# Optimization experiments

Measured on AMD Instinct MI355X. Metric: run time of the kernel, lower is better.

## Reference

```python
import jax, jax.numpy as jnp
import numpy as np

EMB = 1024
HEADS = 16
DH = EMB // HEADS


def setup_inputs() -> dict:
    key = jax.random.key(0)
    ks = jax.random.split(key, 9)
    B, S = 4, 2048
    scale = 1.0 / np.sqrt(EMB)
    x = jax.random.normal(ks[0], (B, S, EMB), dtype=jnp.float32)
    Wq = jax.random.normal(ks[1], (EMB, EMB), dtype=jnp.float32) * scale
    Wk = jax.random.normal(ks[2], (EMB, EMB), dtype=jnp.float32) * scale
    Wv = jax.random.normal(ks[3], (EMB, EMB), dtype=jnp.float32) * scale
    Wo = jax.random.normal(ks[4], (EMB, EMB), dtype=jnp.float32) * scale
    bq = jnp.zeros((EMB,), jnp.float32)
    bk = jnp.zeros((EMB,), jnp.float32)
    bv = jnp.zeros((EMB,), jnp.float32)
    bo = jnp.zeros((EMB,), jnp.float32)
    return {"x": x, "Wq": Wq, "bq": bq, "Wk": Wk, "bk": bk,
            "Wv": Wv, "bv": bv, "Wo": Wo, "bo": bo}


def _split_heads(t):
    B, S, _ = t.shape
    return t.reshape(B, S, HEADS, DH).transpose(0, 2, 1, 3)  # [B,H,S,Dh]


def reference(x, Wq, bq, Wk, bk, Wv, bv, Wo, bo):
    q = _split_heads(x @ Wq + bq)
    k = _split_heads(x @ Wk + bk)
    v = _split_heads(x @ Wv + bv)
    # scaled dot-product attention, full [B,H,S,S] score matrix as in source
    logits = jnp.einsum("bhqd,bhkd->bhqk", q, k) / jnp.sqrt(jnp.float32(DH))
    attn = jax.nn.softmax(logits, axis=-1)
    ctx = jnp.einsum("bhqk,bhkd->bhqd", attn, v)
    B, _, S, _ = ctx.shape
    concat = ctx.transpose(0, 2, 1, 3).reshape(B, S, EMB)
    return concat @ Wo + bo
```

## Files before the change

### kernel.cpp

```cpp
#include <hip/hip_runtime.h>
#include <hip/hip_bf16.h>
#include <stdint.h>

typedef __bf16 bf16;
typedef __bf16 bf16x4 __attribute__((ext_vector_type(4)));
typedef __bf16 bf16x8 __attribute__((ext_vector_type(8)));
typedef float f32x4 __attribute__((ext_vector_type(4)));

__device__ __forceinline__ void async_ld16(const void* g, void* l) {
  __builtin_amdgcn_global_load_lds(
      (__attribute__((address_space(1))) void*)(void*)(g),
      (__attribute__((address_space(3))) void*)(l), 16, 0, 0);
}

__device__ __forceinline__ bf16 fast_bf16(float f) {
  uint32_t u = (__float_as_uint(f) + 0x8000u) >> 16;
  union { uint16_t s; bf16 b; } cv;
  cv.s = (uint16_t)u;
  return cv.b;
}

__device__ __forceinline__ uint32_t pack_bf16(float lo, float hi) {
  return __builtin_amdgcn_perm(__float_as_uint(hi) + 0x8000u,
                               __float_as_uint(lo) + 0x8000u, 0x07060302u);
}

__global__ __launch_bounds__(256) void cast_f32_bf16(const float* __restrict__ in,
                                                     bf16* __restrict__ out, int n) {
  int i = (blockIdx.x * 256 + threadIdx.x) * 4;
  if (i < n) {
    float4 f = *(const float4*)(in + i);
    uint2 o;
    o.x = pack_bf16(f.x, f.y);
    o.y = pack_bf16(f.z, f.w);
    *(uint2*)(out + i) = o;
  }
}

__global__ __launch_bounds__(256) void transpose_weights(const float* __restrict__ Wq,
                                                         const float* __restrict__ Wk,
                                                         const float* __restrict__ Wv,
                                                         const float* __restrict__ Wo,
                                                         bf16* __restrict__ Wt,
                                                         bf16* __restrict__ Wot) {
  __shared__ bf16 tile[64][66];
  int z = blockIdx.z;
  const float* src = z == 0 ? Wq : (z == 1 ? Wk : (z == 2 ? Wv : Wo));
  bf16* dst = z == 0 ? Wt : (z == 1 ? Wt + 1048576 : (z == 2 ? Wt + 2097152 : Wot));
  int r0 = blockIdx.x * 64, c0 = blockIdx.y * 64;
  int t = threadIdx.x;
#pragma unroll
  for (int i = 0; i < 16; ++i) {
    int idx = t + i * 256;
    int r = idx >> 6, c = idx & 63;
    tile[r][c] = fast_bf16(src[(size_t)(r0 + r) * 1024 + (c0 + c)]);
  }
  __syncthreads();
#pragma unroll
  for (int i = 0; i < 16; ++i) {
    int idx = t + i * 256;
    int c = idx >> 6, r = idx & 63;
    dst[(size_t)(c0 + c) * 1024 + (r0 + r)] = tile[r][c];
  }
}

__device__ __forceinline__ void gemm128_mainloop(const bf16* __restrict__ A,
                                                 const bf16* __restrict__ Bt, int K,
                                                 int rowBase, int colBase,
                                                 bf16* As, bf16* Bs,
                                                 f32x4 (&acc)[4][4]) {
  int t = threadIdx.x, lane = t & 63, w = t >> 6;
  int wM = w >> 1, wN = w & 1, quad = lane >> 4, l15 = lane & 15;
  int r_off = lane >> 3;
  int c_sw = (((lane & 7) ^ r_off) << 3);
  int sw = l15 & 7;
  for (int k0 = 0; k0 < K; k0 += 64) {
    __syncthreads();
#pragma unroll
    for (int i = 0; i < 4; ++i) {
      int e = i * 2048 + w * 512;
      int row = (e >> 6) + r_off;
      async_ld16(A + (size_t)(rowBase + row) * K + (k0 + c_sw), As + e);
      async_ld16(Bt + (size_t)(colBase + row) * K + (k0 + c_sw), Bs + e);
    }
    __syncthreads();
#pragma unroll
    for (int ks = 0; ks < 2; ++ks) {
      int co = (((ks * 4 + quad) ^ sw) << 3);
      bf16x8 af[4], bfr[4];
#pragma unroll
      for (int mi = 0; mi < 4; ++mi)
        af[mi] = *(const bf16x8*)(As + (wM * 64 + mi * 16 + l15) * 64 + co);
#pragma unroll
      for (int ni = 0; ni < 4; ++ni)
        bfr[ni] = *(const bf16x8*)(Bs + (wN * 64 + ni * 16 + l15) * 64 + co);
#pragma unroll
      for (int mi = 0; mi < 4; ++mi)
#pragma unroll
        for (int ni = 0; ni < 4; ++ni)
          acc[mi][ni] = __builtin_amdgcn_mfma_f32_16x16x32_bf16(af[mi], bfr[ni], acc[mi][ni], 0, 0, 0);
    }
  }
}

__global__ __launch_bounds__(256) void gemm_qkv(const bf16* __restrict__ X,
                                                const bf16* __restrict__ Wt,
                                                const float* __restrict__ bq,
                                                const float* __restrict__ bk,
                                                const float* __restrict__ bv,
                                                bf16* __restrict__ Qo,
                                                bf16* __restrict__ Ko,
                                                bf16* __restrict__ Vto) {
  __shared__ alignas(16) bf16 smem[2 * 128 * 64];
  bf16* As = smem;
  bf16* Bs = smem + 128 * 64;
  f32x4 acc[4][4];
  f32x4 z = {0.f, 0.f, 0.f, 0.f};
#pragma unroll
  for (int mi = 0; mi < 4; ++mi)
#pragma unroll
    for (int ni = 0; ni < 4; ++ni) acc[mi][ni] = z;
  int rowBase = blockIdx.x * 128, colBase = blockIdx.y * 128;
  gemm128_mainloop(X, Wt, 1024, rowBase, colBase, As, Bs, acc);

  int t = threadIdx.x, lane = t & 63, w = t >> 6;
  int wM = w >> 1, wN = w & 1, quad = lane >> 4, l15 = lane & 15;
  int which = colBase >> 10;

  if (which == 2) {
    int baseh = (colBase & 1023) >> 6;
    int b = rowBase >> 11, s0 = rowBase & 2047;
#pragma unroll
    for (int hp = 0; hp < 2; ++hp) {
      __syncthreads();
      if (wN == hp) {
#pragma unroll
        for (int mi = 0; mi < 4; ++mi)
#pragma unroll
          for (int ni = 0; ni < 4; ++ni) {
            int d = ni * 16 + l15;
            float bb = bv[(colBase & 1023) + hp * 64 + d];
            int sl = wM * 64 + mi * 16 + quad * 4;
            uint2 pv;
            pv.x = pack_bf16(acc[mi][ni][0] + bb, acc[mi][ni][1] + bb);
            pv.y = pack_bf16(acc[mi][ni][2] + bb, acc[mi][ni][3] + bb);
            *(uint2*)(smem + d * 136 + sl) = pv;
          }
      }
      __syncthreads();
      int hg = baseh + hp;
#pragma unroll
      for (int it = 0; it < 4; ++it) {
        int idx = t + it * 256;
        int d = idx >> 4, c = idx & 15;
        bf16x8 vv = *(const bf16x8*)(smem + d * 136 + c * 8);
        *(bf16x8*)(Vto + (((size_t)((b << 4) + hg) << 6) + d) * 2048 + s0 + c * 8) = vv;
      }
    }
  } else {
    const float* bias = which == 0 ? bq : bk;
    bf16* dst = which == 0 ? Qo : Ko;
    float scale = which == 0 ? 0.125f * 1.44269504f : 1.0f;
#pragma unroll
    for (int mi = 0; mi < 4; ++mi)
#pragma unroll
      for (int ni = 0; ni < 4; ++ni) {
        int n = colBase + wN * 64 + ni * 16 + l15;
        int e = n & 1023;
        int h = e >> 6, d = e & 63;
        float bb = bias[e];
#pragma unroll
        for (int r = 0; r < 4; ++r) {
          int m = rowBase + wM * 64 + mi * 16 + quad * 4 + r;
          int b = m >> 11, s = m & 2047;
          dst[(((size_t)((b << 4) + h) * 2048 + s) << 6) + d] =
              fast_bf16((acc[mi][ni][r] + bb) * scale);
        }
      }
  }
}

__global__ __launch_bounds__(256) void gemm_out(const bf16* __restrict__ Cb,
                                                const bf16* __restrict__ Wot,
                                                const float* __restrict__ bo,
                                                float* __restrict__ out) {
  __shared__ alignas(16) bf16 As[128 * 64];
  __shared__ alignas(16) bf16 Bs[128 * 64];
  f32x4 acc[4][4];
  f32x4 z = {0.f, 0.f, 0.f, 0.f};
#pragma unroll
  for (int mi = 0; mi < 4; ++mi)
#pragma unroll
    for (int ni = 0; ni < 4; ++ni) acc[mi][ni] = z;
  int rowBase = blockIdx.x * 128, colBase = blockIdx.y * 128;
  gemm128_mainloop(Cb, Wot, 1024, rowBase, colBase, As, Bs, acc);

  int t = threadIdx.x, lane = t & 63, w = t >> 6;
  int wM = w >> 1, wN = w & 1, quad = lane >> 4, l15 = lane & 15;
#pragma unroll
  for (int mi = 0; mi < 4; ++mi)
#pragma unroll
    for (int ni = 0; ni < 4; ++ni) {
      int n = colBase + wN * 64 + ni * 16 + l15;
      float bb = bo[n];
#pragma unroll
      for (int r = 0; r < 4; ++r) {
        int m = rowBase + wM * 64 + mi * 16 + quad * 4 + r;
        out[(size_t)m * 1024 + n] = acc[mi][ni][r] + bb;
      }
    }
}

__global__ __launch_bounds__(256, 2) void attn(const bf16* __restrict__ Q,
                                               const bf16* __restrict__ Kg,
                                               const bf16* __restrict__ Vt,
                                               bf16* __restrict__ ctx) {
  __shared__ alignas(16) bf16 KVs[4][4096];
  __shared__ alignas(16) bf16 Ps[4][2048];

  int t = threadIdx.x, lane = t & 63, w = t >> 6;
  int quad = lane >> 4, l15 = lane & 15;
  int r_off = lane >> 3;
  int c_sw = (((lane & 7) ^ r_off) << 3);
  int sw = l15 & 7;
  int bh = blockIdx.y;
  int q0 = blockIdx.x * 256;
  const bf16* Qp = Q + ((size_t)bh * 2048 + q0) * 64;
  const bf16* Kp = Kg + (size_t)bh * 2048 * 64;
  const bf16* Vp = Vt + (size_t)bh * 64 * 2048;

#pragma unroll
  for (int i = 0; i < 8; ++i) {
    int e = i * 512;
    int row = i * 8 + r_off;
    async_ld16(Qp + (size_t)(w * 64 + row) * 64 + c_sw, KVs[w] + e);
  }
  __syncthreads();

  bf16x8 qf[2][4];
#pragma unroll
  for (int ks = 0; ks < 2; ++ks)
#pragma unroll
    for (int qi = 0; qi < 4; ++qi)
      qf[ks][qi] = *(const bf16x8*)(KVs[w] + (qi * 16 + l15) * 64 + (((ks * 4 + quad) ^ sw) << 3));
  __syncthreads();

#pragma unroll
  for (int i = 0; i < 2; ++i) {
    int e = w * 1024 + i * 512;
    int row = (e >> 6) + r_off;
    async_ld16(Kp + (size_t)row * 64 + c_sw, KVs[0] + e);
    async_ld16(Vp + (size_t)row * 2048 + c_sw, KVs[2] + e);
  }

  bf16 one1 = (bf16)1.0f;
  bf16x8 ones = {one1, one1, one1, one1, one1, one1, one1, one1};
  bf16* Pw = Ps[w];

  f32x4 o[4][4];
  f32x4 ol[4];
  f32x4 z = {0.f, 0.f, 0.f, 0.f};
#pragma unroll
  for (int mi = 0; mi < 4; ++mi) {
    ol[mi] = z;
#pragma unroll
    for (int ni = 0; ni < 4; ++ni) o[mi][ni] = z;
  }

  for (int kt = 0; kt < 32; ++kt) {
    int cur = kt & 1;
    __syncthreads();
    if (kt < 31) {
      int kn = (kt + 1) * 64;
#pragma unroll
      for (int i = 0; i < 2; ++i) {
        int e = w * 1024 + i * 512;
        int row = (e >> 6) + r_off;
        async_ld16(Kp + (size_t)(kn + row) * 64 + c_sw, KVs[cur ^ 1] + e);
        async_ld16(Vp + (size_t)row * 2048 + kn + c_sw, KVs[2 + (cur ^ 1)] + e);
      }
    }
    const bf16* Kc = KVs[cur];
    const bf16* Vc = KVs[2 + cur];

    f32x4 sA[2][4];
#pragma unroll
    for (int ki = 0; ki < 2; ++ki)
#pragma unroll
      for (int qi = 0; qi < 4; ++qi) sA[ki][qi] = z;
#pragma unroll
    for (int ks = 0; ks < 2; ++ks) {
      int co = (((ks * 4 + quad) ^ sw) << 3);
      bf16x8 kf0 = *(const bf16x8*)(Kc + (l15)*64 + co);
      bf16x8 kf1 = *(const bf16x8*)(Kc + (16 + l15) * 64 + co);
#pragma unroll
      for (int qi = 0; qi < 4; ++qi) {
        sA[0][qi] = __builtin_amdgcn_mfma_f32_16x16x32_bf16(kf0, qf[ks][qi], sA[0][qi], 0, 0, 0);
        sA[1][qi] = __builtin_amdgcn_mfma_f32_16x16x32_bf16(kf1, qf[ks][qi], sA[1][qi], 0, 0, 0);
      }
    }
#pragma unroll
    for (int qi = 0; qi < 4; ++qi)
#pragma unroll
      for (int ki = 0; ki < 2; ++ki) {
        float p0 = __builtin_amdgcn_exp2f(sA[ki][qi][0]);
        float p1 = __builtin_amdgcn_exp2f(sA[ki][qi][1]);
        float p2 = __builtin_amdgcn_exp2f(sA[ki][qi][2]);
        float p3 = __builtin_amdgcn_exp2f(sA[ki][qi][3]);
        uint2 pb;
        pb.x = pack_bf16(p0, p1);
        pb.y = pack_bf16(p2, p3);
        *(uint2*)(Pw + (qi * 16 + l15) * 32 + ki * 16 + quad * 4) = pb;
      }

    f32x4 sB[2][4];
#pragma unroll
    for (int ki = 0; ki < 2; ++ki)
#pragma unroll
      for (int qi = 0; qi < 4; ++qi) sB[ki][qi] = z;
#pragma unroll
    for (int ks = 0; ks < 2; ++ks) {
      int co = (((ks * 4 + quad) ^ sw) << 3);
      bf16x8 kf2 = *(const bf16x8*)(Kc + (32 + l15) * 64 + co);
      bf16x8 kf3 = *(const bf16x8*)(Kc + (48 + l15) * 64 + co);
#pragma unroll
      for (int qi = 0; qi < 4; ++qi) {
        sB[0][qi] = __builtin_amdgcn_mfma_f32_16x16x32_bf16(kf2, qf[ks][qi], sB[0][qi], 0, 0, 0);
        sB[1][qi] = __builtin_amdgcn_mfma_f32_16x16x32_bf16(kf3, qf[ks][qi], sB[1][qi], 0, 0, 0);
      }
    }

    asm volatile("s_waitcnt lgkmcnt(0)" ::: "memory");

    {
      int co = ((quad ^ sw) << 3);
      bf16x8 pf[4], vf[4];
#pragma unroll
      for (int mi = 0; mi < 4; ++mi)
        pf[mi] = *(const bf16x8*)(Pw + (mi * 16 + l15) * 32 + quad * 8);
#pragma unroll
      for (int ni = 0; ni < 4; ++ni)
        vf[ni] = *(const bf16x8*)(Vc + (ni * 16 + l15) * 64 + co);
#pragma unroll
      for (int mi = 0; mi < 4; ++mi) {
#pragma unroll
        for (int ni = 0; ni < 4; ++ni)
          o[mi][ni] = __builtin_amdgcn_mfma_f32_16x16x32_bf16(pf[mi], vf[ni], o[mi][ni], 0, 0, 0);
        ol[mi] = __builtin_amdgcn_mfma_f32_16x16x32_bf16(pf[mi], ones, ol[mi], 0, 0, 0);
      }
    }

#pragma unroll
    for (int qi = 0; qi < 4; ++qi)
#pragma unroll
      for (int ki = 0; ki < 2; ++ki) {
        float p0 = __builtin_amdgcn_exp2f(sB[ki][qi][0]);
        float p1 = __builtin_amdgcn_exp2f(sB[ki][qi][1]);
        float p2 = __builtin_amdgcn_exp2f(sB[ki][qi][2]);
        float p3 = __builtin_amdgcn_exp2f(sB[ki][qi][3]);
        uint2 pb;
        pb.x = pack_bf16(p0, p1);
        pb.y = pack_bf16(p2, p3);
        *(uint2*)(Pw + (qi * 16 + l15) * 32 + ki * 16 + quad * 4) = pb;
      }

    asm volatile("s_waitcnt lgkmcnt(0)" ::: "memory");

    {
      int co = (((4 + quad) ^ sw) << 3);
      bf16x8 pf[4], vf[4];
#pragma unroll
      for (int mi = 0; mi < 4; ++mi)
        pf[mi] = *(const bf16x8*)(Pw + (mi * 16 + l15) * 32 + quad * 8);
#pragma unroll
      for (int ni = 0; ni < 4; ++ni)
        vf[ni] = *(const bf16x8*)(Vc + (ni * 16 + l15) * 64 + co);
#pragma unroll
      for (int mi = 0; mi < 4; ++mi) {
#pragma unroll
        for (int ni = 0; ni < 4; ++ni)
          o[mi][ni] = __builtin_amdgcn_mfma_f32_16x16x32_bf16(pf[mi], vf[ni], o[mi][ni], 0, 0, 0);
        ol[mi] = __builtin_amdgcn_mfma_f32_16x16x32_bf16(pf[mi], ones, ol[mi], 0, 0, 0);
      }
    }
  }

  int b = bh >> 4, h = bh & 15;
#pragma unroll
  for (int mi = 0; mi < 4; ++mi) {
    float rl[4];
#pragma unroll
    for (int r = 0; r < 4; ++r) rl[r] = 1.0f / ol[mi][r];
#pragma unroll
    for (int ni = 0; ni < 4; ++ni) {
      int col = h * 64 + ni * 16 + l15;
#pragma unroll
      for (int r = 0; r < 4; ++r) {
        int q = q0 + w * 64 + mi * 16 + quad * 4 + r;
        ctx[(size_t)(b * 2048 + q) * 1024 + col] = fast_bf16(o[mi][ni][r] * rl[r]);
      }
    }
  }
}

extern "C" void kernel_launch(void* const* d_in, const int* in_sizes, int n_in,
                              void* d_out, int out_size, void* d_ws, size_t ws_size,
                              hipStream_t stream) {
  const float* x  = (const float*)d_in[0];
  const float* Wq = (const float*)d_in[1];
  const float* bq = (const float*)d_in[2];
  const float* Wk = (const float*)d_in[3];
  const float* bk = (const float*)d_in[4];
  const float* Wv = (const float*)d_in[5];
  const float* bv = (const float*)d_in[6];
  const float* Wo = (const float*)d_in[7];
  const float* bo = (const float*)d_in[8];
  float* out = (float*)d_out;

  char* ws = (char*)d_ws;
  const size_t MB = 1048576;
  bf16* xb  = (bf16*)(ws);
  bf16* Wt  = (bf16*)(ws + 16 * MB);
  bf16* Wot = (bf16*)(ws + 22 * MB);
  bf16* Qb  = (bf16*)(ws + 24 * MB);
  bf16* Kb  = (bf16*)(ws + 40 * MB);
  bf16* Vtb = (bf16*)(ws + 56 * MB);
  bf16* Cx  = (bf16*)(ws + 72 * MB);

  cast_f32_bf16<<<8192, 256, 0, stream>>>(x, xb, 8388608);
  transpose_weights<<<dim3(16, 16, 4), 256, 0, stream>>>(Wq, Wk, Wv, Wo, Wt, Wot);
  gemm_qkv<<<dim3(64, 24, 1), 256, 0, stream>>>(xb, Wt, bq, bk, bv, Qb, Kb, Vtb);
  attn<<<dim3(8, 64, 1), 256, 0, stream>>>(Qb, Kb, Vtb, Cx);
  gemm_out<<<dim3(64, 8, 1), 256, 0, stream>>>(Cx, Wot, bo, out);
}
```

Baseline: 310.7 us.

## Stage Q/K epilogue through LDS, swap grid order, restructure attention LDS

The Q/K GEMM epilogue now stages each head tile in shared memory and writes 16-byte vectorized rows, replacing scattered 2-byte stores. All three kernels swap grid axes so consecutive blocks share the same row or head tile, which should improve L2 reuse. The attention kernel reuses the Q staging buffer for P with an XOR swizzle, loads the first K/V tile together with Q, and moves the per-iteration barrier to the end of the loop. LDS per block grows slightly, and occupancy may change.

```diff
diff --git a/kernel.cpp b/kernel.cpp
--- a/kernel.cpp
+++ b/kernel.cpp
@@ -120,16 +120,16 @@
   for (int mi = 0; mi < 4; ++mi)
 #pragma unroll
     for (int ni = 0; ni < 4; ++ni) acc[mi][ni] = z;
-  int rowBase = blockIdx.x * 128, colBase = blockIdx.y * 128;
+  int rowBase = blockIdx.y * 128, colBase = blockIdx.x * 128;
   gemm128_mainloop(X, Wt, 1024, rowBase, colBase, As, Bs, acc);
 
   int t = threadIdx.x, lane = t & 63, w = t >> 6;
   int wM = w >> 1, wN = w & 1, quad = lane >> 4, l15 = lane & 15;
   int which = colBase >> 10;
+  int baseh = (colBase & 1023) >> 6;
+  int b = rowBase >> 11, s0 = rowBase & 2047;
 
   if (which == 2) {
-    int baseh = (colBase & 1023) >> 6;
-    int b = rowBase >> 11, s0 = rowBase & 2047;
 #pragma unroll
     for (int hp = 0; hp < 2; ++hp) {
       __syncthreads();
@@ -162,21 +162,32 @@
     bf16* dst = which == 0 ? Qo : Ko;
     float scale = which == 0 ? 0.125f * 1.44269504f : 1.0f;
 #pragma unroll
-    for (int mi = 0; mi < 4; ++mi)
-#pragma unroll
-      for (int ni = 0; ni < 4; ++ni) {
-        int n = colBase + wN * 64 + ni * 16 + l15;
-        int e = n & 1023;
-        int h = e >> 6, d = e & 63;
-        float bb = bias[e];
-#pragma unroll
-        for (int r = 0; r < 4; ++r) {
-          int m = rowBase + wM * 64 + mi * 16 + quad * 4 + r;
-          int b = m >> 11, s = m & 2047;
-          dst[(((size_t)((b << 4) + h) * 2048 + s) << 6) + d] =
-              fast_bf16((acc[mi][ni][r] + bb) * scale);
-        }
-      }
+    for (int hp = 0; hp < 2; ++hp) {
+      __syncthreads();
+      if (wN == hp) {
+#pragma unroll
+        for (int mi = 0; mi < 4; ++mi)
+#pragma unroll
+          for (int ni = 0; ni < 4; ++ni) {
+            int d = ni * 16 + l15;
+            float bb = bias[(colBase & 1023) + hp * 64 + d];
+            int m = wM * 64 + mi * 16 + quad * 4;
+#pragma unroll
+            for (int r = 0; r < 4; ++r)
+              smem[(m + r) * 72 + d] = fast_bf16((acc[mi][ni][r] + bb) * scale);
+          }
+      }
+      __syncthreads();
+      int hg = baseh + hp;
+      bf16* gbase = dst + ((((size_t)((b << 4) + hg)) * 2048 + s0) << 6);
+#pragma unroll
+      for (int it = 0; it < 4; ++it) {
+        int idx = t + it * 256;
+        int m = idx >> 3, c = idx & 7;
+        bf16x8 vv = *(const bf16x8*)(smem + m * 72 + c * 8);
+        *(bf16x8*)(gbase + m * 64 + c * 8) = vv;
+      }
+    }
   }
 }
 
@@ -192,7 +203,7 @@
   for (int mi = 0; mi < 4; ++mi)
 #pragma unroll
     for (int ni = 0; ni < 4; ++ni) acc[mi][ni] = z;
-  int rowBase = blockIdx.x * 128, colBase = blockIdx.y * 128;
+  int rowBase = blockIdx.y * 128, colBase = blockIdx.x * 128;
   gemm128_mainloop(Cb, Wot, 1024, rowBase, colBase, As, Bs, acc);
 
   int t = threadIdx.x, lane = t & 63, w = t >> 6;
@@ -215,47 +226,48 @@
                                                const bf16* __restrict__ Kg,
                                                const bf16* __restrict__ Vt,
                                                bf16* __restrict__ ctx) {
-  __shared__ alignas(16) bf16 KVs[4][4096];
-  __shared__ alignas(16) bf16 Ps[4][2048];
+  __shared__ alignas(16) bf16 QPs[256 * 64];
+  __shared__ alignas(16) bf16 Ks[2][4096];
+  __shared__ alignas(16) bf16 Vs[2][4096];
 
   int t = threadIdx.x, lane = t & 63, w = t >> 6;
   int quad = lane >> 4, l15 = lane & 15;
   int r_off = lane >> 3;
   int c_sw = (((lane & 7) ^ r_off) << 3);
   int sw = l15 & 7;
-  int bh = blockIdx.y;
-  int q0 = blockIdx.x * 256;
+  int bh = blockIdx.x;
+  int q0 = blockIdx.y * 256;
   const bf16* Qp = Q + ((size_t)bh * 2048 + q0) * 64;
   const bf16* Kp = Kg + (size_t)bh * 2048 * 64;
   const bf16* Vp = Vt + (size_t)bh * 64 * 2048;
 
 #pragma unroll
   for (int i = 0; i < 8; ++i) {
-    int e = i * 512;
-    int row = i * 8 + r_off;
-    async_ld16(Qp + (size_t)(w * 64 + row) * 64 + c_sw, KVs[w] + e);
-  }
-  __syncthreads();
-
-  bf16x8 qf[2][4];
-#pragma unroll
-  for (int ks = 0; ks < 2; ++ks)
-#pragma unroll
-    for (int qi = 0; qi < 4; ++qi)
-      qf[ks][qi] = *(const bf16x8*)(KVs[w] + (qi * 16 + l15) * 64 + (((ks * 4 + quad) ^ sw) << 3));
-  __syncthreads();
-
+    int e = w * 4096 + i * 512;
+    int row = (e >> 6) + r_off;
+    async_ld16(Qp + (size_t)row * 64 + c_sw, QPs + e);
+  }
 #pragma unroll
   for (int i = 0; i < 2; ++i) {
     int e = w * 1024 + i * 512;
     int row = (e >> 6) + r_off;
-    async_ld16(Kp + (size_t)row * 64 + c_sw, KVs[0] + e);
-    async_ld16(Vp + (size_t)row * 2048 + c_sw, KVs[2] + e);
-  }
+    async_ld16(Kp + (size_t)row * 64 + c_sw, Ks[0] + e);
+    async_ld16(Vp + (size_t)row * 2048 + c_sw, Vs[0] + e);
+  }
+  __syncthreads();
+
+  bf16x8 qf[2][4];
+#pragma unroll
+  for (int ks = 0; ks < 2; ++ks)
+#pragma unroll
+    for (int qi = 0; qi < 4; ++qi)
+      qf[ks][qi] = *(const bf16x8*)(QPs + (w * 64 + qi * 16 + l15) * 64 + (((ks * 4 + quad) ^ sw) << 3));
+  asm volatile("s_waitcnt lgkmcnt(0)" ::: "memory");
+
+  bf16* Ps = QPs + w * 4096;
 
   bf16 one1 = (bf16)1.0f;
   bf16x8 ones = {one1, one1, one1, one1, one1, one1, one1, one1};
-  bf16* Pw = Ps[w];
 
   f32x4 o[4][4];
   f32x4 ol[4];
@@ -269,19 +281,18 @@
 
   for (int kt = 0; kt < 32; ++kt) {
     int cur = kt & 1;
-    __syncthreads();
     if (kt < 31) {
       int kn = (kt + 1) * 64;
 #pragma unroll
       for (int i = 0; i < 2; ++i) {
         int e = w * 1024 + i * 512;
         int row = (e >> 6) + r_off;
-        async_ld16(Kp + (size_t)(kn + row) * 64 + c_sw, KVs[cur ^ 1] + e);
-        async_ld16(Vp + (size_t)row * 2048 + kn + c_sw, KVs[2 + (cur ^ 1)] + e);
-      }
-    }
-    const bf16* Kc = KVs[cur];
-    const bf16* Vc = KVs[2 + cur];
+        async_ld16(Kp + (size_t)(kn + row) * 64 + c_sw, Ks[cur ^ 1] + e);
+        async_ld16(Vp + (size_t)row * 2048 + kn + c_sw, Vs[cur ^ 1] + e);
+      }
+    }
+    const bf16* Kc = Ks[cur];
+    const bf16* Vc = Vs[cur];
 
     f32x4 sA[2][4];
 #pragma unroll
@@ -291,7 +302,7 @@
 #pragma unroll
     for (int ks = 0; ks < 2; ++ks) {
       int co = (((ks * 4 + quad) ^ sw) << 3);
-      bf16x8 kf0 = *(const bf16x8*)(Kc + (l15)*64 + co);
+      bf16x8 kf0 = *(const bf16x8*)(Kc + (l15) * 64 + co);
       bf16x8 kf1 = *(const bf16x8*)(Kc + (16 + l15) * 64 + co);
 #pragma unroll
       for (int qi = 0; qi < 4; ++qi) {
@@ -310,7 +321,8 @@
         uint2 pb;
         pb.x = pack_bf16(p0, p1);
         pb.y = pack_bf16(p2, p3);
-        *(uint2*)(Pw + (qi * 16 + l15) * 32 + ki * 16 + quad * 4) = pb;
+        int cs = (ki * 2 + (quad >> 1)) ^ sw;
+        *(uint2*)(Ps + (qi * 16 + l15) * 64 + cs * 8 + (quad & 1) * 4) = pb;
       }
 
     f32x4 sB[2][4];
@@ -337,7 +349,7 @@
       bf16x8 pf[4], vf[4];
 #pragma unroll
       for (int mi = 0; mi < 4; ++mi)
-        pf[mi] = *(const bf16x8*)(Pw + (mi * 16 + l15) * 32 + quad * 8);
+        pf[mi] = *(const bf16x8*)(Ps + (mi * 16 + l15) * 64 + co);
 #pragma unroll
       for (int ni = 0; ni < 4; ++ni)
         vf[ni] = *(const bf16x8*)(Vc + (ni * 16 + l15) * 64 + co);
@@ -361,7 +373,8 @@
         uint2 pb;
         pb.x = pack_bf16(p0, p1);
         pb.y = pack_bf16(p2, p3);
-        *(uint2*)(Pw + (qi * 16 + l15) * 32 + ki * 16 + quad * 4) = pb;
+        int cs = (ki * 2 + 4 + (quad >> 1)) ^ sw;
+        *(uint2*)(Ps + (qi * 16 + l15) * 64 + cs * 8 + (quad & 1) * 4) = pb;
       }
 
     asm volatile("s_waitcnt lgkmcnt(0)" ::: "memory");
@@ -371,7 +384,7 @@
       bf16x8 pf[4], vf[4];
 #pragma unroll
       for (int mi = 0; mi < 4; ++mi)
-        pf[mi] = *(const bf16x8*)(Pw + (mi * 16 + l15) * 32 + quad * 8);
+        pf[mi] = *(const bf16x8*)(Ps + (mi * 16 + l15) * 64 + co);
 #pragma unroll
       for (int ni = 0; ni < 4; ++ni)
         vf[ni] = *(const bf16x8*)(Vc + (ni * 16 + l15) * 64 + co);
@@ -383,6 +396,8 @@
         ol[mi] = __builtin_amdgcn_mfma_f32_16x16x32_bf16(pf[mi], ones, ol[mi], 0, 0, 0);
       }
     }
+
+    __syncthreads();
   }
 
   int b = bh >> 4, h = bh & 15;
@@ -429,7 +444,7 @@
 
   cast_f32_bf16<<<8192, 256, 0, stream>>>(x, xb, 8388608);
   transpose_weights<<<dim3(16, 16, 4), 256, 0, stream>>>(Wq, Wk, Wv, Wo, Wt, Wot);
-  gemm_qkv<<<dim3(64, 24, 1), 256, 0, stream>>>(xb, Wt, bq, bk, bv, Qb, Kb, Vtb);
-  attn<<<dim3(8, 64, 1), 256, 0, stream>>>(Qb, Kb, Vtb, Cx);
-  gemm_out<<<dim3(64, 8, 1), 256, 0, stream>>>(Cx, Wot, bo, out);
-}
+  gemm_qkv<<<dim3(24, 64, 1), 256, 0, stream>>>(xb, Wt, bq, bk, bv, Qb, Kb, Vtb);
+  attn<<<dim3(64, 8, 1), 256, 0, stream>>>(Qb, Kb, Vtb, Cx);
+  gemm_out<<<dim3(8, 64, 1), 256, 0, stream>>>(Cx, Wot, bo, out);
+}
```

Result: faster. 276.2 us (-11.1%).
